# Kernel tuning notes

Hardware: AMD Instinct MI355X
Metric: run time of the kernel (lower is better)

Reference implementation:

```python
import jax, jax.numpy as jnp
import numpy as np

DIM = 1024
NUM_HEADS = 16
HEAD_DIM = 64  # DIM // NUM_HEADS
BATCH = 2
SEQ = 2048


def setup_inputs() -> dict:
    key = jax.random.key(0)
    ks = jax.random.split(key, 6)
    x = jax.random.normal(ks[0], (BATCH, SEQ, DIM), dtype=jnp.float32)
    # Linear weights stored as [in, out] so y = x @ W (same math as torch Linear).
    Wq = jax.random.normal(ks[1], (DIM, DIM), dtype=jnp.float32) * (DIM ** -0.5)
    # MQA: single shared KV head of size HEAD_DIM.
    Wk = jax.random.normal(ks[2], (DIM, HEAD_DIM), dtype=jnp.float32) * (DIM ** -0.5)
    Wv = jax.random.normal(ks[3], (DIM, HEAD_DIM), dtype=jnp.float32) * (DIM ** -0.5)
    Wo = jax.random.normal(ks[4], (DIM, DIM), dtype=jnp.float32) * (DIM ** -0.5)
    bo = jax.random.normal(ks[5], (DIM,), dtype=jnp.float32) * 0.01
    return {"x": x, "Wq": Wq, "Wk": Wk, "Wv": Wv, "Wo": Wo, "bo": bo}


def reference(x, Wq, Wk, Wv, Wo, bo):
    b, s, _ = x.shape
    scale = HEAD_DIM ** -0.5
    # Per-head queries [b, h, s, d]
    q = (x @ Wq).reshape(b, s, NUM_HEADS, HEAD_DIM).transpose(0, 2, 1, 3) * scale
    # Shared single KV head [b, s, d]
    k = x @ Wk
    v = x @ Wv
    # Materialized scores [b, h, s_q, s_k]
    scores = jnp.einsum('bhqd,bkd->bhqk', q, k)
    causal = jnp.tril(jnp.ones((s, s), dtype=bool))  # True where allowed
    scores = jnp.where(causal, scores, -jnp.inf)
    # Manual stable softmax (max, exp, sum, div) as in the original
    max_scores = jnp.max(scores, axis=-1, keepdims=True)
    exp_scores = jnp.exp(scores - max_scores)
    attn = exp_scores / jnp.sum(exp_scores, axis=-1, keepdims=True)
    out = jnp.einsum('bhqk,bkd->bhqd', attn, v)  # [b, h, s, d]
    out = out.transpose(0, 2, 1, 3).reshape(b, s, DIM)
    return out @ Wo + bo
```

## Files before the change

kernel.cpp:

```cpp
#include <hip/hip_runtime.h>

typedef unsigned short u16;
typedef __attribute__((ext_vector_type(8))) short short8;
typedef __attribute__((ext_vector_type(4))) float f32x4;

static __device__ __forceinline__ u16 f32_to_bf16(float f) {
  unsigned u = __float_as_uint(f);
  u += 0x7fffu + ((u >> 16) & 1u);
  return (u16)(u >> 16);
}

static __device__ __forceinline__ void async16(u16* lds, const u16* g) {
  __builtin_amdgcn_global_load_lds(
      (const __attribute__((address_space(1))) void*)g,
      (__attribute__((address_space(3))) void*)lds, 16, 0, 0);
}


__global__ void __launch_bounds__(256) prep_kernel(
    const float* __restrict__ x,
    const float* __restrict__ Wq, const float* __restrict__ Wk,
    const float* __restrict__ Wv, const float* __restrict__ Wo,
    u16* __restrict__ Xb, u16* __restrict__ WqT, u16* __restrict__ WkvT,
    u16* __restrict__ WoT) {
  __shared__ u16 T[64][72];
  int id = blockIdx.x;
  int tid = threadIdx.x;
  if (id < 2048) {
    int base = (id * 256 + tid) * 8;
    float4 a = *(const float4*)&x[base];
    float4 b = *(const float4*)&x[base + 4];
    short8 v;
    v[0] = (short)f32_to_bf16(a.x); v[1] = (short)f32_to_bf16(a.y);
    v[2] = (short)f32_to_bf16(a.z); v[3] = (short)f32_to_bf16(a.w);
    v[4] = (short)f32_to_bf16(b.x); v[5] = (short)f32_to_bf16(b.y);
    v[6] = (short)f32_to_bf16(b.z); v[7] = (short)f32_to_bf16(b.w);
    *(short8*)&Xb[base] = v;
    return;
  }
  int id2 = id - 2048;
  const float* src; u16* dst; int tk, tn, src_ld, row_off;
  if (id2 < 256)      { src = Wq; dst = WqT;  tk = id2 & 15; tn = id2 >> 4; src_ld = 1024; row_off = 0; }
  else if (id2 < 512) { int i = id2 - 256; src = Wo; dst = WoT; tk = i & 15; tn = i >> 4; src_ld = 1024; row_off = 0; }
  else if (id2 < 528) { src = Wk; dst = WkvT; tk = id2 - 512; tn = 0; src_ld = 64; row_off = 0; }
  else                { src = Wv; dst = WkvT; tk = id2 - 528; tn = 0; src_ld = 64; row_off = 64; }
  int k0 = tk * 64, n0 = tn * 64;
#pragma unroll
  for (int it = 0; it < 2; ++it) {
    int c = tid + it * 256;
    int r = c >> 3, cc = (c & 7) * 8;
    const float* p = &src[(k0 + r) * src_ld + n0 + cc];
    float4 a = *(const float4*)&p[0];
    float4 b = *(const float4*)&p[4];
    short8 v;
    v[0] = (short)f32_to_bf16(a.x); v[1] = (short)f32_to_bf16(a.y);
    v[2] = (short)f32_to_bf16(a.z); v[3] = (short)f32_to_bf16(a.w);
    v[4] = (short)f32_to_bf16(b.x); v[5] = (short)f32_to_bf16(b.y);
    v[6] = (short)f32_to_bf16(b.z); v[7] = (short)f32_to_bf16(b.w);
    *(short8*)&T[r][cc] = v;
  }
  __syncthreads();
#pragma unroll
  for (int it = 0; it < 2; ++it) {
    int c = tid + it * 256;
    int r = c >> 3, cc = (c & 7) * 8;
    short8 v;
#pragma unroll
    for (int j = 0; j < 8; ++j) v[j] = (short)T[cc + j][r];
    *(short8*)&dst[(row_off + n0 + r) * 1024 + k0 + cc] = v;
  }
}

__device__ __forceinline__ void gemm_core_64x128(
    const u16* __restrict__ A, const u16* __restrict__ BT, int m0, int K,
    f32x4 (&acc)[2][4], u16* As, u16* Bs,
    int lane, int w, int wr, int wc, int g, int lo) {
  int lrow = lane >> 3;
  int swz8 = ((lane & 7) ^ lrow) * 8;
  int lo7 = lo & 7;
  for (int k0 = 0; k0 < K; k0 += 64) {
#pragma unroll
    for (int it = 0; it < 2; ++it) {
      int W = w * 2 + it;
      async16(As + W * 512, &A[(size_t)(m0 + W * 8 + lrow) * K + k0 + swz8]);
    }
#pragma unroll
    for (int it = 0; it < 4; ++it) {
      int W = w * 4 + it;
      async16(Bs + W * 512, &BT[(size_t)(W * 8 + lrow) * K + k0 + swz8]);
    }
    __syncthreads();
#pragma unroll
    for (int ks = 0; ks < 2; ++ks) {
      int pc = ((ks * 4 + g) ^ lo7) * 8;
      short8 af[2], bf[4];
#pragma unroll
      for (int i = 0; i < 2; ++i)
        af[i] = *(const short8*)&As[(wr * 32 + i * 16 + lo) * 64 + pc];
#pragma unroll
      for (int i = 0; i < 4; ++i)
        bf[i] = *(const short8*)&Bs[(wc * 64 + i * 16 + lo) * 64 + pc];
#pragma unroll
      for (int mi = 0; mi < 2; ++mi)
#pragma unroll
        for (int ni = 0; ni < 4; ++ni)
          acc[mi][ni] = __builtin_amdgcn_mfma_f32_16x16x32_bf16(
              af[mi], bf[ni], acc[mi][ni], 0, 0, 0);
    }
    __syncthreads();
  }
}

__global__ void __launch_bounds__(256) qkv_gemm(
    const u16* __restrict__ Xb, const u16* __restrict__ WqT,
    const u16* __restrict__ WkvT, u16* __restrict__ Qb, u16* __restrict__ KVb,
    u16* __restrict__ VTb) {
  __shared__ u16 As[64 * 64];
  __shared__ u16 Bs[128 * 64];
  int tid = threadIdx.x, lane = tid & 63, w = tid >> 6;
  int wr = w >> 1, wc = w & 1, g = lane >> 4, lo = lane & 15;
  int m0 = blockIdx.x * 64, nb = blockIdx.y;
  const u16* BT = (nb < 8) ? (WqT + (size_t)nb * 128 * 1024) : WkvT;
  f32x4 acc[2][4];
  f32x4 zz = {0.f, 0.f, 0.f, 0.f};
#pragma unroll
  for (int i = 0; i < 2; ++i)
#pragma unroll
    for (int j = 0; j < 4; ++j) acc[i][j] = zz;
  gemm_core_64x128(Xb, BT, m0, 1024, acc, As, Bs, lane, w, wr, wc, g, lo);
#pragma unroll
  for (int mi = 0; mi < 2; ++mi)
#pragma unroll
    for (int ni = 0; ni < 4; ++ni)
#pragma unroll
      for (int r = 0; r < 4; ++r) {
        int row = m0 + wr * 32 + mi * 16 + g * 4 + r;
        int col = wc * 64 + ni * 16 + lo;
        u16 v = f32_to_bf16(acc[mi][ni][r]);
        if (nb < 8) {
          Qb[row * 1024 + nb * 128 + col] = v;
        } else if (wc == 0) {
          KVb[row * 64 + col] = v;
        } else {
          int d = col - 64;
          VTb[(((row >> 11) * 64) + d) * 2048 + (row & 2047)] = v;
        }
      }
}

__global__ void __launch_bounds__(256, 4) attn_kernel(
    const u16* __restrict__ Qb, const u16* __restrict__ KVb,
    const u16* __restrict__ VTb, u16* __restrict__ AOb) {
  __shared__ u16 Ks[64 * 64];
  __shared__ u16 Vt[64 * 64];
  __shared__ u16 Ps[4][16][72];
  int tid = threadIdx.x, lane = tid & 63, w = tid >> 6;
  int g = lane >> 4, lo = lane & 15;
  int h = blockIdx.x;
  int by = blockIdx.y;
  int qt = (by < 16) ? by : (47 - by);
  int b = blockIdx.z;
  int q0 = qt * 64;
  int qbase = q0 + w * 16;
  int lrow = lane >> 3;
  int swz8 = ((lane & 7) ^ lrow) * 8;
  int lo7 = lo & 7;

  short8 qf[2];
  {
    const u16* qp = &Qb[(size_t)(b * 2048 + qbase + lo) * 1024 + h * 64];
    qf[0] = *(const short8*)&qp[g * 8];
    qf[1] = *(const short8*)&qp[32 + g * 8];
  }

  short8 ones;
#pragma unroll
  for (int j = 0; j < 8; ++j) ones[j] = (short)0x3F80;

  f32x4 oacc[4], l_acc;
  f32x4 zz = {0.f, 0.f, 0.f, 0.f};
#pragma unroll
  for (int i = 0; i < 4; ++i) oacc[i] = zz;
  l_acc = zz;

  const float kExp = 0.18033688011112042f;
  const float kOff = 11.541560327111707f;

  int ntiles = qt + 1;
  for (int t = 0; t < ntiles; ++t) {
    int k0 = t * 64;
#pragma unroll
    for (int it = 0; it < 2; ++it) {
      int W = w * 2 + it;
      async16(Ks + W * 512, &KVb[(size_t)(b * 2048 + k0 + W * 8 + lrow) * 64 + swz8]);
      async16(Vt + W * 512, &VTb[((size_t)b * 64 + W * 8 + lrow) * 2048 + k0 + swz8]);
    }
    __syncthreads();

    f32x4 sacc[4];
#pragma unroll
    for (int ns = 0; ns < 4; ++ns) sacc[ns] = zz;
#pragma unroll
    for (int ks = 0; ks < 2; ++ks) {
      short8 kf[4];
      int pc = ((ks * 4 + g) ^ lo7) * 8;
#pragma unroll
      for (int ns = 0; ns < 4; ++ns)
        kf[ns] = *(const short8*)&Ks[(ns * 16 + lo) * 64 + pc];
#pragma unroll
      for (int ns = 0; ns < 4; ++ns)
        sacc[ns] = __builtin_amdgcn_mfma_f32_16x16x32_bf16(
            qf[ks], kf[ns], sacc[ns], 0, 0, 0);
    }

    bool need_mask = (k0 + 63) > qbase;
#pragma unroll
    for (int ns = 0; ns < 4; ++ns)
#pragma unroll
      for (int r = 0; r < 4; ++r) {
        float p = __builtin_amdgcn_exp2f(fmaf(sacc[ns][r], kExp, -kOff));
        if (need_mask) {
          int qg = qbase + g * 4 + r;
          int kg = k0 + ns * 16 + lo;
          if (kg > qg) p = 0.f;
        }
        Ps[w][g * 4 + r][ns * 16 + lo] = f32_to_bf16(p);
      }
    __threadfence_block();

#pragma unroll
    for (int k2 = 0; k2 < 2; ++k2) {
      short8 pf = *(const short8*)&Ps[w][lo][k2 * 32 + g * 8];
      short8 vf[4];
      int pc = ((k2 * 4 + g) ^ lo7) * 8;
#pragma unroll
      for (int ds = 0; ds < 4; ++ds)
        vf[ds] = *(const short8*)&Vt[(ds * 16 + lo) * 64 + pc];
#pragma unroll
      for (int ds = 0; ds < 4; ++ds)
        oacc[ds] = __builtin_amdgcn_mfma_f32_16x16x32_bf16(
            pf, vf[ds], oacc[ds], 0, 0, 0);
      l_acc = __builtin_amdgcn_mfma_f32_16x16x32_bf16(pf, ones, l_acc, 0, 0, 0);
    }
    __syncthreads();
  }

#pragma unroll
  for (int r = 0; r < 4; ++r) {
    float inv_l = 1.0f / l_acc[r];
    int row = b * 2048 + qbase + g * 4 + r;
#pragma unroll
    for (int ds = 0; ds < 4; ++ds)
      AOb[row * 1024 + h * 64 + ds * 16 + lo] = f32_to_bf16(oacc[ds][r] * inv_l);
  }
}

__global__ void __launch_bounds__(256) out_gemm(
    const u16* __restrict__ A, const u16* __restrict__ WoT,
    const float* __restrict__ bias, float* __restrict__ C) {
  __shared__ u16 As[64 * 64];
  __shared__ u16 Bs[128 * 64];
  int tid = threadIdx.x, lane = tid & 63, w = tid >> 6;
  int wr = w >> 1, wc = w & 1, g = lane >> 4, lo = lane & 15;
  int m0 = blockIdx.x * 64, nb = blockIdx.y;
  const u16* BT = WoT + (size_t)nb * 128 * 1024;
  f32x4 acc[2][4];
  f32x4 zz = {0.f, 0.f, 0.f, 0.f};
#pragma unroll
  for (int i = 0; i < 2; ++i)
#pragma unroll
    for (int j = 0; j < 4; ++j) acc[i][j] = zz;
  gemm_core_64x128(A, BT, m0, 1024, acc, As, Bs, lane, w, wr, wc, g, lo);
#pragma unroll
  for (int mi = 0; mi < 2; ++mi)
#pragma unroll
    for (int ni = 0; ni < 4; ++ni)
#pragma unroll
      for (int r = 0; r < 4; ++r) {
        int row = m0 + wr * 32 + mi * 16 + g * 4 + r;
        int col = nb * 128 + wc * 64 + ni * 16 + lo;
        C[row * 1024 + col] = acc[mi][ni][r] + bias[col];
      }
}

extern "C" void kernel_launch(void* const* d_in, const int* in_sizes, int n_in,
                              void* d_out, int out_size, void* d_ws, size_t ws_size,
                              hipStream_t stream) {
  const float* x  = (const float*)d_in[0];
  const float* Wq = (const float*)d_in[1];
  const float* Wk = (const float*)d_in[2];
  const float* Wv = (const float*)d_in[3];
  const float* Wo = (const float*)d_in[4];
  const float* bo = (const float*)d_in[5];
  float* out = (float*)d_out;

  u16* ws   = (u16*)d_ws;
  u16* AOb  = ws;
  u16* KVb  = AOb + 4194304;
  u16* VTb  = KVb + 262144;
  u16* Xb   = VTb + 262144;
  u16* WqT  = Xb + 4194304;
  u16* WoT  = WqT + 1048576;
  u16* WkvT = WoT + 1048576;
  u16* Qb   = (u16*)d_out;

  prep_kernel<<<2592, 256, 0, stream>>>(x, Wq, Wk, Wv, Wo, Xb, WqT, WkvT, WoT);
  qkv_gemm<<<dim3(64, 9), 256, 0, stream>>>(Xb, WqT, WkvT, Qb, KVb, VTb);
  attn_kernel<<<dim3(16, 32, 2), 256, 0, stream>>>(Qb, KVb, VTb, AOb);
  out_gemm<<<dim3(64, 8), 256, 0, stream>>>(AOb, WoT, bo, out);
}
```

Baseline: 160.4 us.

## Double-buffer GEMM and attention LDS tiles, pair causal query tiles per block

Both GEMM kernels now double-buffer their A/B LDS tiles and prefetch the next K tile asynchronously while the current one is multiplied, which removes one barrier per iteration. The attention kernel pairs a low and a high causal query tile in each block so that each K/V tile loaded serves both, balancing work and halving the grid. K/V staging is also double-buffered. The P-to-bf16 conversion now truncates instead of rounding, and launch bounds drop to 2 waves/EU because more registers and LDS are used.

Result: faster. 156.4 us (-2.5%).

```diff
diff --git a/kernel.cpp b/kernel.cpp
--- a/kernel.cpp
+++ b/kernel.cpp
@@ -71,35 +71,48 @@
   }
 }
 
-__device__ __forceinline__ void gemm_core_64x128(
+__device__ __forceinline__ void stage_64x128(
+    const u16* __restrict__ A, const u16* __restrict__ BT, int m0, int K,
+    int k0, u16* As, u16* Bs, int w, int lrow, int swz8) {
+#pragma unroll
+  for (int it = 0; it < 2; ++it) {
+    int W = w * 2 + it;
+    async16(As + W * 512, &A[(size_t)(m0 + W * 8 + lrow) * K + k0 + swz8]);
+  }
+#pragma unroll
+  for (int it = 0; it < 4; ++it) {
+    int W = w * 4 + it;
+    async16(Bs + W * 512, &BT[(size_t)(W * 8 + lrow) * K + k0 + swz8]);
+  }
+}
+
+__device__ __forceinline__ void gemm_core_64x128_db(
     const u16* __restrict__ A, const u16* __restrict__ BT, int m0, int K,
     f32x4 (&acc)[2][4], u16* As, u16* Bs,
     int lane, int w, int wr, int wc, int g, int lo) {
   int lrow = lane >> 3;
   int swz8 = ((lane & 7) ^ lrow) * 8;
   int lo7 = lo & 7;
-  for (int k0 = 0; k0 < K; k0 += 64) {
-#pragma unroll
-    for (int it = 0; it < 2; ++it) {
-      int W = w * 2 + it;
-      async16(As + W * 512, &A[(size_t)(m0 + W * 8 + lrow) * K + k0 + swz8]);
-    }
-#pragma unroll
-    for (int it = 0; it < 4; ++it) {
-      int W = w * 4 + it;
-      async16(Bs + W * 512, &BT[(size_t)(W * 8 + lrow) * K + k0 + swz8]);
-    }
+  const int NK = K >> 6;
+  stage_64x128(A, BT, m0, K, 0, As, Bs, w, lrow, swz8);
+  for (int kt = 0; kt < NK; ++kt) {
+    int cur = kt & 1;
     __syncthreads();
+    if (kt + 1 < NK)
+      stage_64x128(A, BT, m0, K, (kt + 1) * 64,
+                   As + (cur ^ 1) * 4096, Bs + (cur ^ 1) * 8192, w, lrow, swz8);
+    const u16* Asc = As + cur * 4096;
+    const u16* Bsc = Bs + cur * 8192;
 #pragma unroll
     for (int ks = 0; ks < 2; ++ks) {
       int pc = ((ks * 4 + g) ^ lo7) * 8;
       short8 af[2], bf[4];
 #pragma unroll
       for (int i = 0; i < 2; ++i)
-        af[i] = *(const short8*)&As[(wr * 32 + i * 16 + lo) * 64 + pc];
+        af[i] = *(const short8*)&Asc[(wr * 32 + i * 16 + lo) * 64 + pc];
 #pragma unroll
       for (int i = 0; i < 4; ++i)
-        bf[i] = *(const short8*)&Bs[(wc * 64 + i * 16 + lo) * 64 + pc];
+        bf[i] = *(const short8*)&Bsc[(wc * 64 + i * 16 + lo) * 64 + pc];
 #pragma unroll
       for (int mi = 0; mi < 2; ++mi)
 #pragma unroll
@@ -107,7 +120,6 @@
           acc[mi][ni] = __builtin_amdgcn_mfma_f32_16x16x32_bf16(
               af[mi], bf[ni], acc[mi][ni], 0, 0, 0);
     }
-    __syncthreads();
   }
 }
 
@@ -115,8 +127,8 @@
     const u16* __restrict__ Xb, const u16* __restrict__ WqT,
     const u16* __restrict__ WkvT, u16* __restrict__ Qb, u16* __restrict__ KVb,
     u16* __restrict__ VTb) {
-  __shared__ u16 As[64 * 64];
-  __shared__ u16 Bs[128 * 64];
+  __shared__ u16 As[2 * 64 * 64];
+  __shared__ u16 Bs[2 * 128 * 64];
   int tid = threadIdx.x, lane = tid & 63, w = tid >> 6;
   int wr = w >> 1, wc = w & 1, g = lane >> 4, lo = lane & 15;
   int m0 = blockIdx.x * 64, nb = blockIdx.y;
@@ -127,7 +139,7 @@
   for (int i = 0; i < 2; ++i)
 #pragma unroll
     for (int j = 0; j < 4; ++j) acc[i][j] = zz;
-  gemm_core_64x128(Xb, BT, m0, 1024, acc, As, Bs, lane, w, wr, wc, g, lo);
+  gemm_core_64x128_db(Xb, BT, m0, 1024, acc, As, Bs, lane, w, wr, wc, g, lo);
 #pragma unroll
   for (int mi = 0; mi < 2; ++mi)
 #pragma unroll
@@ -148,118 +160,138 @@
       }
 }
 
-__global__ void __launch_bounds__(256, 4) attn_kernel(
+__global__ void __launch_bounds__(256, 2) attn_kernel(
     const u16* __restrict__ Qb, const u16* __restrict__ KVb,
     const u16* __restrict__ VTb, u16* __restrict__ AOb) {
-  __shared__ u16 Ks[64 * 64];
-  __shared__ u16 Vt[64 * 64];
+  __shared__ u16 Ks[2][64 * 64];
+  __shared__ u16 Vt[2][64 * 64];
   __shared__ u16 Ps[4][16][72];
   int tid = threadIdx.x, lane = tid & 63, w = tid >> 6;
-  int g = lane >> 4, lo = lane & 15;
-  int h = blockIdx.x;
-  int by = blockIdx.y;
-  int qt = (by < 16) ? by : (47 - by);
-  int b = blockIdx.z;
-  int q0 = qt * 64;
-  int qbase = q0 + w * 16;
+  int gq = lane >> 4, lo = lane & 15;
+  int pg = blockIdx.x;
+  int h = blockIdx.y;
+  int z = blockIdx.z;
+  int b = z;
+  int a = z ? (15 - pg) : pg;
+  int hi = 31 - a;
+  int qb_lo = a * 64 + w * 16;
+  int qb_hi = hi * 64 + w * 16;
   int lrow = lane >> 3;
   int swz8 = ((lane & 7) ^ lrow) * 8;
   int lo7 = lo & 7;
 
-  short8 qf[2];
+  short8 qf_lo[2], qf_hi[2];
   {
-    const u16* qp = &Qb[(size_t)(b * 2048 + qbase + lo) * 1024 + h * 64];
-    qf[0] = *(const short8*)&qp[g * 8];
-    qf[1] = *(const short8*)&qp[32 + g * 8];
+    const u16* qp = &Qb[(size_t)(b * 2048 + qb_lo + lo) * 1024 + h * 64];
+    qf_lo[0] = *(const short8*)&qp[gq * 8];
+    qf_lo[1] = *(const short8*)&qp[32 + gq * 8];
+    const u16* qp2 = &Qb[(size_t)(b * 2048 + qb_hi + lo) * 1024 + h * 64];
+    qf_hi[0] = *(const short8*)&qp2[gq * 8];
+    qf_hi[1] = *(const short8*)&qp2[32 + gq * 8];
   }
 
   short8 ones;
 #pragma unroll
   for (int j = 0; j < 8; ++j) ones[j] = (short)0x3F80;
 
-  f32x4 oacc[4], l_acc;
   f32x4 zz = {0.f, 0.f, 0.f, 0.f};
-#pragma unroll
-  for (int i = 0; i < 4; ++i) oacc[i] = zz;
-  l_acc = zz;
+  f32x4 oacc_lo[4], oacc_hi[4], l_lo, l_hi;
+#pragma unroll
+  for (int i = 0; i < 4; ++i) { oacc_lo[i] = zz; oacc_hi[i] = zz; }
+  l_lo = zz; l_hi = zz;
 
   const float kExp = 0.18033688011112042f;
   const float kOff = 11.541560327111707f;
 
-  int ntiles = qt + 1;
-  for (int t = 0; t < ntiles; ++t) {
-    int k0 = t * 64;
-#pragma unroll
-    for (int it = 0; it < 2; ++it) {
-      int W = w * 2 + it;
-      async16(Ks + W * 512, &KVb[(size_t)(b * 2048 + k0 + W * 8 + lrow) * 64 + swz8]);
-      async16(Vt + W * 512, &VTb[((size_t)b * 64 + W * 8 + lrow) * 2048 + k0 + swz8]);
-    }
-    __syncthreads();
-
+  auto do_strip = [&](const short8 (&qf)[2], f32x4 (&oacc)[4], f32x4& l_acc,
+                      int qbase, bool diag, int k0,
+                      const u16* Kc, const u16* Vc) {
     f32x4 sacc[4];
 #pragma unroll
     for (int ns = 0; ns < 4; ++ns) sacc[ns] = zz;
 #pragma unroll
     for (int ks = 0; ks < 2; ++ks) {
+      int pc = ((ks * 4 + gq) ^ lo7) * 8;
       short8 kf[4];
-      int pc = ((ks * 4 + g) ^ lo7) * 8;
 #pragma unroll
       for (int ns = 0; ns < 4; ++ns)
-        kf[ns] = *(const short8*)&Ks[(ns * 16 + lo) * 64 + pc];
+        kf[ns] = *(const short8*)&Kc[(ns * 16 + lo) * 64 + pc];
 #pragma unroll
       for (int ns = 0; ns < 4; ++ns)
         sacc[ns] = __builtin_amdgcn_mfma_f32_16x16x32_bf16(
             qf[ks], kf[ns], sacc[ns], 0, 0, 0);
     }
-
-    bool need_mask = (k0 + 63) > qbase;
 #pragma unroll
     for (int ns = 0; ns < 4; ++ns)
 #pragma unroll
       for (int r = 0; r < 4; ++r) {
         float p = __builtin_amdgcn_exp2f(fmaf(sacc[ns][r], kExp, -kOff));
-        if (need_mask) {
-          int qg = qbase + g * 4 + r;
+        if (diag) {
+          int qg = qbase + gq * 4 + r;
           int kg = k0 + ns * 16 + lo;
           if (kg > qg) p = 0.f;
         }
-        Ps[w][g * 4 + r][ns * 16 + lo] = f32_to_bf16(p);
+        Ps[w][gq * 4 + r][ns * 16 + lo] = (u16)(__float_as_uint(p) >> 16);
       }
     __threadfence_block();
-
 #pragma unroll
     for (int k2 = 0; k2 < 2; ++k2) {
-      short8 pf = *(const short8*)&Ps[w][lo][k2 * 32 + g * 8];
+      short8 pf = *(const short8*)&Ps[w][lo][k2 * 32 + gq * 8];
+      int pc = ((k2 * 4 + gq) ^ lo7) * 8;
       short8 vf[4];
-      int pc = ((k2 * 4 + g) ^ lo7) * 8;
 #pragma unroll
       for (int ds = 0; ds < 4; ++ds)
-        vf[ds] = *(const short8*)&Vt[(ds * 16 + lo) * 64 + pc];
+        vf[ds] = *(const short8*)&Vc[(ds * 16 + lo) * 64 + pc];
 #pragma unroll
       for (int ds = 0; ds < 4; ++ds)
         oacc[ds] = __builtin_amdgcn_mfma_f32_16x16x32_bf16(
             pf, vf[ds], oacc[ds], 0, 0, 0);
       l_acc = __builtin_amdgcn_mfma_f32_16x16x32_bf16(pf, ones, l_acc, 0, 0, 0);
     }
+  };
+
+  auto stage_kv = [&](int t, int bu) {
+#pragma unroll
+    for (int it = 0; it < 2; ++it) {
+      int W = w * 2 + it;
+      async16(&Ks[bu][W * 512],
+              &KVb[(size_t)(b * 2048 + t * 64 + W * 8 + lrow) * 64 + swz8]);
+      async16(&Vt[bu][W * 512],
+              &VTb[((size_t)b * 64 + W * 8 + lrow) * 2048 + t * 64 + swz8]);
+    }
+  };
+
+  int nst = hi + 1;
+  stage_kv(0, 0);
+  for (int t = 0; t < nst; ++t) {
+    int cur = t & 1;
     __syncthreads();
+    if (t + 1 < nst) stage_kv(t + 1, cur ^ 1);
+    int k0 = t * 64;
+    do_strip(qf_hi, oacc_hi, l_hi, qb_hi, t == hi, k0, Ks[cur], Vt[cur]);
+    if (t <= a)
+      do_strip(qf_lo, oacc_lo, l_lo, qb_lo, t == a, k0, Ks[cur], Vt[cur]);
   }
 
 #pragma unroll
   for (int r = 0; r < 4; ++r) {
-    float inv_l = 1.0f / l_acc[r];
-    int row = b * 2048 + qbase + g * 4 + r;
-#pragma unroll
-    for (int ds = 0; ds < 4; ++ds)
-      AOb[row * 1024 + h * 64 + ds * 16 + lo] = f32_to_bf16(oacc[ds][r] * inv_l);
+    float inv_lo = 1.0f / l_lo[r];
+    float inv_hi = 1.0f / l_hi[r];
+    int row_lo = b * 2048 + qb_lo + gq * 4 + r;
+    int row_hi = b * 2048 + qb_hi + gq * 4 + r;
+#pragma unroll
+    for (int ds = 0; ds < 4; ++ds) {
+      AOb[row_lo * 1024 + h * 64 + ds * 16 + lo] = f32_to_bf16(oacc_lo[ds][r] * inv_lo);
+      AOb[row_hi * 1024 + h * 64 + ds * 16 + lo] = f32_to_bf16(oacc_hi[ds][r] * inv_hi);
+    }
   }
 }
 
 __global__ void __launch_bounds__(256) out_gemm(
     const u16* __restrict__ A, const u16* __restrict__ WoT,
     const float* __restrict__ bias, float* __restrict__ C) {
-  __shared__ u16 As[64 * 64];
-  __shared__ u16 Bs[128 * 64];
+  __shared__ u16 As[2 * 64 * 64];
+  __shared__ u16 Bs[2 * 128 * 64];
   int tid = threadIdx.x, lane = tid & 63, w = tid >> 6;
   int wr = w >> 1, wc = w & 1, g = lane >> 4, lo = lane & 15;
   int m0 = blockIdx.x * 64, nb = blockIdx.y;
@@ -270,7 +302,7 @@
   for (int i = 0; i < 2; ++i)
 #pragma unroll
     for (int j = 0; j < 4; ++j) acc[i][j] = zz;
-  gemm_core_64x128(A, BT, m0, 1024, acc, As, Bs, lane, w, wr, wc, g, lo);
+  gemm_core_64x128_db(A, BT, m0, 1024, acc, As, Bs, lane, w, wr, wc, g, lo);
 #pragma unroll
   for (int mi = 0; mi < 2; ++mi)
 #pragma unroll
@@ -306,6 +338,6 @@
 
   prep_kernel<<<2592, 256, 0, stream>>>(x, Wq, Wk, Wv, Wo, Xb, WqT, WkvT, WoT);
   qkv_gemm<<<dim3(64, 9), 256, 0, stream>>>(Xb, WqT, WkvT, Qb, KVb, VTb);
-  attn_kernel<<<dim3(16, 32, 2), 256, 0, stream>>>(Qb, KVb, VTb, AOb);
+  attn_kernel<<<dim3(16, 16, 2), 256, 0, stream>>>(Qb, KVb, VTb, AOb);
   out_gemm<<<dim3(64, 8), 256, 0, stream>>>(AOb, WoT, bo, out);
 }
```
